# Kernel tuning notes

Measured on AMD Instinct MI355X. Metric: run time of the kernel, lower is better.

The kernel has to match this reference:

```python
import jax, jax.numpy as jnp
import numpy as np
from math import ceil, log2

LEVELS = 6
N = 4096
DB4 = np.array([0.23037781330885523, 0.7148465705525415, 0.6308807679295904,
                -0.02798376941698385, -0.18703481171888114, 0.030841381835986965,
                0.032883011666982945, -0.010597401784997278], dtype=np.float32)


def setup_inputs() -> dict:
    key = jax.random.key(0)
    x = jax.random.normal(key, (N, N), dtype=jnp.float32)
    # learned filter bank: scaling.repeat(levels*2, 1)
    scaling = jnp.tile(jnp.asarray(DB4), (LEVELS * 2, 1))
    return {
        "x": x,
        "scaling": scaling,
        "alpha": jnp.float32(10.0),
        "b_plus": jnp.float32(2.0),
        "b_minus": jnp.float32(1.0),
    }


def compute_wavelet(h):
    # g_k = flip(h); odd indices negated
    g = jnp.flip(h, -1)
    sign = jnp.where(jnp.arange(g.shape[-1]) % 2 == 1, -1.0, 1.0).astype(g.dtype)
    return g * sign


def convolve(x, f, transpose=False):
    # circular convolution (or correlation if transpose) along last axis via FFT,
    # exactly as torch rfft/irfft with n=input_length
    L = x.shape[-1]
    fa = jnp.fft.rfft(x, axis=-1)
    fb = jnp.fft.rfft(f, n=L)
    if transpose:
        fb = jnp.conj(fb)
    return jnp.fft.irfft(fa * fb, n=L, axis=-1)


def forward_layer(x, h):
    w = compute_wavelet(h)
    return convolve(x, w)[:, ::2], convolve(x, h)[:, ::2]


def backward_layer(d, a, h):
    w = compute_wavelet(h)
    fd = jnp.zeros((d.shape[0], d.shape[1] * 2), d.dtype).at[:, ::2].set(d)
    fa = jnp.zeros((a.shape[0], a.shape[1] * 2), a.dtype).at[:, ::2].set(a)
    return convolve(fd, w, transpose=True) + convolve(fa, h, transpose=True)


def forward2d(x, hH, hV):
    d, a = forward_layer(x, hH)
    hh, hl = forward_layer(d.T, hV)
    hh, hl = hh.T, hl.T
    lh, ll = forward_layer(a.T, hV)
    lh, ll = lh.T, ll.T
    return (hh, hl, lh), ll


def backward2d(hh, hl, lh, ll, hH, hV):
    h = backward_layer(hh.T, hl.T, hV).T
    l = backward_layer(lh.T, ll.T, hV).T
    return backward_layer(h, l, hH)


def _despawn(x, scaling, alpha, b_plus, b_minus):
    n, m = x.shape
    pn = 2 ** ceil(log2(n)) - n
    pm = 2 ** ceil(log2(m)) - m
    xp = jnp.pad(x, ((0, pn), (0, pm)), mode="edge") if (pn or pm) else x

    approx = xp
    coeffs = []
    for lev in range(LEVELS):
        dets, approx = forward2d(approx, scaling[lev], scaling[lev + 1])
        coeffs.append(dets)

    def thr(t):
        return t * (jax.nn.sigmoid(alpha * (t - b_plus)) + jax.nn.sigmoid(-alpha * (t + b_minus)))

    filt = [tuple(thr(c) for c in tup) for tup in coeffs] + [thr(approx)]

    a = filt[-1]
    for lev in reversed(range(LEVELS)):
        hh, hl, lh = filt[lev]
        a = backward2d(hh, hl, lh, a, scaling[lev], scaling[lev + 1])

    flat = jnp.concatenate(
        [jnp.concatenate(tup, axis=-1).reshape(-1) for tup in filt[:-1]]
        + [filt[-1].reshape(-1)]
    )
    return a[:n, :m], flat


def reference(x, scaling, alpha, b_plus, b_minus):
    return _despawn(x, scaling, alpha, b_plus, b_minus)
```

## Files before the change

### kernel.cpp

```cpp
#include <hip/hip_runtime.h>


__device__ __forceinline__ float thrf(float t, float alpha, float bp, float bm) {
    float s1 = 1.0f / (1.0f + __expf(-alpha * (t - bp)));
    float s2 = 1.0f / (1.0f + __expf( alpha * (t + bm)));
    return t * (s1 + s2);
}

__device__ __forceinline__ void load_filt(const float* __restrict__ filt,
                                          float (&h)[8], float (&w)[8]) {
#pragma unroll
    for (int k = 0; k < 8; ++k) h[k] = filt[k];
#pragma unroll
    for (int k = 0; k < 8; ++k) w[k] = (k & 1) ? -h[7 - k] : h[7 - k];
}

__global__ __launch_bounds__(256) void fwd_fused(
    const float* __restrict__ X, int s, int sh,
    float* __restrict__ flat, float* __restrict__ All,
    const float* __restrict__ filt_row, const float* __restrict__ filt_col,
    const float* __restrict__ ap, const float* __restrict__ bpp,
    const float* __restrict__ bmp) {
    __shared__ __align__(16) float xs[70][72];
    __shared__ __align__(16) float Ds[70][36];
    __shared__ __align__(16) float As[70][36];
    const int tid = threadIdx.x;
    const int j0 = blockIdx.x * 32, i0 = blockIdx.y * 32;
    float hr[8], wr[8], hc[8], wc[8];
    load_filt(filt_row, hr, wr);
    load_filt(filt_col, hc, wc);
    const int sm = s - 1;

    for (int idx = tid; idx < 70 * 18; idx += 256) {
        int rr = idx / 18, c = idx - rr * 18;
        int gr = (2 * i0 - 7 + rr) & sm;
        int gc = (2 * j0 - 8 + 4 * c) & sm;
        *(float4*)&xs[rr][4 * c] = *(const float4*)&X[(size_t)gr * s + gc];
    }
    __syncthreads();

    for (int idx = tid; idx < 70 * 8; idx += 256) {
        int rr = idx >> 3, q = idx & 7;
        const float4* xr = (const float4*)&xs[rr][8 * q];
        float wv[16];
#pragma unroll
        for (int m = 0; m < 4; ++m) {
            float4 t = xr[m];
            wv[4 * m + 0] = t.x; wv[4 * m + 1] = t.y;
            wv[4 * m + 2] = t.z; wv[4 * m + 3] = t.w;
        }
        float d[4], a[4];
#pragma unroll
        for (int e = 0; e < 4; ++e) {
            float dd = 0.f, aa = 0.f;
#pragma unroll
            for (int u = 0; u < 8; ++u) {
                float v = wv[2 * e + 1 + u];
                dd += wr[7 - u] * v;
                aa += hr[7 - u] * v;
            }
            d[e] = dd; a[e] = aa;
        }
        *(float4*)&Ds[rr][4 * q] = make_float4(d[0], d[1], d[2], d[3]);
        *(float4*)&As[rr][4 * q] = make_float4(a[0], a[1], a[2], a[3]);
    }
    __syncthreads();

    const float alpha = *ap, bp = *bpp, bm = *bmp;
    {
        const int j = tid & 31, iq = tid >> 5;
        float Dw[14], Aw[14];
#pragma unroll
        for (int t = 0; t < 14; ++t) {
            Dw[t] = Ds[8 * iq + t][j];
            Aw[t] = As[8 * iq + t][j];
        }
#pragma unroll
        for (int e = 0; e < 4; ++e) {
            float hh = 0.f, hl = 0.f, lh = 0.f, ll = 0.f;
#pragma unroll
            for (int u = 0; u < 8; ++u) {
                float dv = Dw[2 * e + u], av = Aw[2 * e + u];
                hh += wc[7 - u] * dv;
                hl += hc[7 - u] * dv;
                lh += wc[7 - u] * av;
                ll += hc[7 - u] * av;
            }
            int row = i0 + 4 * iq + e;
            size_t ro = (size_t)row * (3 * sh) + (j0 + j);
            flat[ro]           = thrf(hh, alpha, bp, bm);
            flat[ro + sh]      = thrf(hl, alpha, bp, bm);
            flat[ro + 2 * sh]  = thrf(lh, alpha, bp, bm);
            All[(size_t)row * sh + (j0 + j)] = ll;
        }
    }
}

__global__ void thr_kernel(const float* __restrict__ in, float* __restrict__ out,
                           int n, const float* __restrict__ ap,
                           const float* __restrict__ bpp,
                           const float* __restrict__ bmp) {
    int idx = blockIdx.x * blockDim.x + threadIdx.x;
    if (idx >= n) return;
    out[idx] = thrf(in[idx], *ap, *bpp, *bmp);
}

__global__ __launch_bounds__(256) void inv_fused(
    const float* __restrict__ flatl, const float* __restrict__ a, int astride,
    int sc, float* __restrict__ outp, int ostride,
    const float* __restrict__ filt_col, const float* __restrict__ filt_row) {
    __shared__ __align__(16) float hhs[36][36], hls[36][36], lhs[36][36], as_[36][36];
    __shared__ __align__(16) float Hs[64][36], Ls[64][36];
    const int tid = threadIdx.x;
    const int m0 = blockIdx.x * 64, i0 = blockIdx.y * 64;
    float hr[8], wr[8], hc[8], wc[8];
    load_filt(filt_row, hr, wr);
    load_filt(filt_col, hc, wc);
    const int mm = sc - 1;
    const int r0 = i0 >> 1, c0 = m0 >> 1;
    const int ds = 3 * sc;

    for (int idx = tid; idx < 4 * 324; idx += 256) {
        int aid = idx / 324, rem = idx - aid * 324;
        int rr = rem / 9, c = rem - rr * 9;
        int gr = (r0 + rr) & mm;
        int gc = (c0 + 4 * c) & mm;
        if (aid == 0)
            *(float4*)&hhs[rr][4 * c] = *(const float4*)&flatl[(size_t)gr * ds + gc];
        else if (aid == 1)
            *(float4*)&hls[rr][4 * c] = *(const float4*)&flatl[(size_t)gr * ds + sc + gc];
        else if (aid == 2)
            *(float4*)&lhs[rr][4 * c] = *(const float4*)&flatl[(size_t)gr * ds + 2 * sc + gc];
        else
            *(float4*)&as_[rr][4 * c] = *(const float4*)&a[(size_t)gr * astride + gc];
    }
    __syncthreads();

    for (int idx = tid; idx < 16 * 36; idx += 256) {
        int q = idx / 36, jj = idx - q * 36;
        float hv[6], lv[6], gv[6], av[6];
#pragma unroll
        for (int d = 0; d < 6; ++d) {
            int lr = 2 * q + d;
            hv[d] = hhs[lr][jj];
            lv[d] = hls[lr][jj];
            gv[d] = lhs[lr][jj];
            av[d] = as_[lr][jj];
        }
        float H0 = 0.f, H1 = 0.f, H2 = 0.f, H3 = 0.f;
        float L0 = 0.f, L1 = 0.f, L2 = 0.f, L3 = 0.f;
#pragma unroll
        for (int t = 0; t < 4; ++t) {
            float we = wc[2 * t], he = hc[2 * t];
            float wo = wc[2 * t + 1], ho = hc[2 * t + 1];
            H0 += we * hv[t]     + he * lv[t];
            H1 += wo * hv[t + 1] + ho * lv[t + 1];
            H2 += we * hv[t + 1] + he * lv[t + 1];
            H3 += wo * hv[t + 2] + ho * lv[t + 2];
            L0 += we * gv[t]     + he * av[t];
            L1 += wo * gv[t + 1] + ho * av[t + 1];
            L2 += we * gv[t + 1] + he * av[t + 1];
            L3 += wo * gv[t + 2] + ho * av[t + 2];
        }
        Hs[4 * q + 0][jj] = H0; Hs[4 * q + 1][jj] = H1;
        Hs[4 * q + 2][jj] = H2; Hs[4 * q + 3][jj] = H3;
        Ls[4 * q + 0][jj] = L0; Ls[4 * q + 1][jj] = L1;
        Ls[4 * q + 2][jj] = L2; Ls[4 * q + 3][jj] = L3;
    }
    __syncthreads();

    for (int idx = tid; idx < 64 * 16; idx += 256) {
        int i = idx >> 4, p = idx & 15;
        const float2* hp = (const float2*)&Hs[i][2 * p];
        const float2* lp = (const float2*)&Ls[i][2 * p];
        float2 hA = hp[0], hB = hp[1], hC = hp[2];
        float2 lA = lp[0], lB = lp[1], lC = lp[2];
        float Hw[6] = {hA.x, hA.y, hB.x, hB.y, hC.x, hC.y};
        float Lw[6] = {lA.x, lA.y, lB.x, lB.y, lC.x, lC.y};
        float o0 = 0.f, o1 = 0.f, o2 = 0.f, o3 = 0.f;
#pragma unroll
        for (int t = 0; t < 4; ++t) {
            float we = wr[2 * t], he = hr[2 * t];
            float wo = wr[2 * t + 1], ho = hr[2 * t + 1];
            o0 += we * Hw[t]     + he * Lw[t];
            o1 += wo * Hw[t + 1] + ho * Lw[t + 1];
            o2 += we * Hw[t + 1] + he * Lw[t + 1];
            o3 += wo * Hw[t + 2] + ho * Lw[t + 2];
        }
        *(float4*)&outp[(size_t)(i0 + i) * ostride + (m0 + 4 * p)] =
            make_float4(o0, o1, o2, o3);
    }
}

extern "C" void kernel_launch(void* const* d_in, const int* in_sizes, int n_in,
                              void* d_out, int out_size, void* d_ws, size_t ws_size,
                              hipStream_t stream) {
    const float* x    = (const float*)d_in[0];
    const float* scal = (const float*)d_in[1];
    const float* ap   = (const float*)d_in[2];
    const float* bp   = (const float*)d_in[3];
    const float* bm   = (const float*)d_in[4];
    float* out = (float*)d_out;
    float* ws  = (float*)d_ws;

    const int N = 4096;
    float* recon = out;
    float* flat  = out + 16777216;

    static const size_t Aoff[7] = {0, 0, 4194304, 5242880, 5505024, 5570560, 5586944};
    static const size_t flatOff[6] = {0, 12582912, 15728640, 16515072, 16711680, 16760832};
    const size_t finalOff = 16773120;
    float* P0 = ws + 5591040;
    float* P1 = ws + 5591040 + 4194304;

    dim3 blk(256);

    const float* src = x;
    for (int lev = 0; lev < 6; ++lev) {
        int s = N >> lev, sh = s >> 1;
        dim3 g(sh / 32, sh / 32);
        fwd_fused<<<g, blk, 0, stream>>>(src, s, sh, flat + flatOff[lev],
                                         ws + Aoff[lev + 1],
                                         scal + lev * 8, scal + (lev + 1) * 8,
                                         ap, bp, bm);
        src = ws + Aoff[lev + 1];
    }
    thr_kernel<<<dim3(16), blk, 0, stream>>>(ws + Aoff[6], flat + finalOff, 4096,
                                             ap, bp, bm);

    const float* a_in = flat + finalOff;
    for (int lev = 5; lev >= 0; --lev) {
        int sc = N >> (lev + 1), r = 2 * sc;
        float* outp = (lev == 0) ? recon : ((lev & 1) ? P1 : P0);
        dim3 g(r / 64, r / 64);
        inv_fused<<<g, blk, 0, stream>>>(flat + flatOff[lev], a_in, sc,
                                         sc, outp, r,
                                         scal + (lev + 1) * 8, scal + lev * 8);
        a_in = outp;
    }
}
```

Baseline: 307.0 us.

## Drop input shared-memory staging, fuse final threshold, split passes to cut registers

Both kernels now read their input windows straight from global memory instead of staging them in shared memory. This shrinks LDS use, and __launch_bounds__(256,8) is added to raise occupancy. The column passes are split into two halves so fewer register arrays are live at once. Wavelet coefficients are derived inline from h rather than kept in separate registers, and the final-approx threshold is folded into the last forward kernel, which removes one launch. The cost is redundant global/L2 reads of overlapping halos and less-coalesced scalar loads in the inverse kernel.

```diff
diff --git a/kernel.cpp b/kernel.cpp
--- a/kernel.cpp
+++ b/kernel.cpp
@@ -7,45 +7,30 @@
     return t * (s1 + s2);
 }
 
-__device__ __forceinline__ void load_filt(const float* __restrict__ filt,
-                                          float (&h)[8], float (&w)[8]) {
+__device__ __forceinline__ void load_h(const float* __restrict__ filt,
+                                       float (&h)[8]) {
 #pragma unroll
     for (int k = 0; k < 8; ++k) h[k] = filt[k];
-#pragma unroll
-    for (int k = 0; k < 8; ++k) w[k] = (k & 1) ? -h[7 - k] : h[7 - k];
-}
-
-__global__ __launch_bounds__(256) void fwd_fused(
-    const float* __restrict__ X, int s, int sh,
-    float* __restrict__ flat, float* __restrict__ All,
-    const float* __restrict__ filt_row, const float* __restrict__ filt_col,
-    const float* __restrict__ ap, const float* __restrict__ bpp,
-    const float* __restrict__ bmp) {
-    __shared__ __align__(16) float xs[70][72];
-    __shared__ __align__(16) float Ds[70][36];
-    __shared__ __align__(16) float As[70][36];
-    const int tid = threadIdx.x;
-    const int j0 = blockIdx.x * 32, i0 = blockIdx.y * 32;
-    float hr[8], wr[8], hc[8], wc[8];
-    load_filt(filt_row, hr, wr);
-    load_filt(filt_col, hc, wc);
-    const int sm = s - 1;
-
-    for (int idx = tid; idx < 70 * 18; idx += 256) {
-        int rr = idx / 18, c = idx - rr * 18;
-        int gr = (2 * i0 - 7 + rr) & sm;
-        int gc = (2 * j0 - 8 + 4 * c) & sm;
-        *(float4*)&xs[rr][4 * c] = *(const float4*)&X[(size_t)gr * s + gc];
-    }
-    __syncthreads();
-
+}
+
+struct SMemF { float Ds[70][36]; float As[70][36]; };
+struct SMemI { float Hs[64][36]; float Ls[64][36]; };
+
+__device__ __forceinline__ void fwd_tile(
+    SMemF& sm, const float* __restrict__ X, int s, int sh,
+    float* __restrict__ flat, float* __restrict__ All, bool thr_ll,
+    const float (&h)[8], const float (&g)[8],
+    float alpha, float bp, float bm, int i0, int j0, int tid) {
+    const int smk = s - 1;
     for (int idx = tid; idx < 70 * 8; idx += 256) {
         int rr = idx >> 3, q = idx & 7;
-        const float4* xr = (const float4*)&xs[rr][8 * q];
+        int gr = (2 * i0 - 7 + rr) & smk;
+        const float* xrow = X + (size_t)gr * s;
+        int cbase = 2 * j0 - 8 + 8 * q;
         float wv[16];
 #pragma unroll
         for (int m = 0; m < 4; ++m) {
-            float4 t = xr[m];
+            float4 t = *(const float4*)&xrow[(cbase + 4 * m) & smk];
             wv[4 * m + 0] = t.x; wv[4 * m + 1] = t.y;
             wv[4 * m + 2] = t.z; wv[4 * m + 3] = t.w;
         }
@@ -56,123 +41,116 @@
 #pragma unroll
             for (int u = 0; u < 8; ++u) {
                 float v = wv[2 * e + 1 + u];
-                dd += wr[7 - u] * v;
-                aa += hr[7 - u] * v;
+                aa += h[7 - u] * v;
+                dd += (u & 1) ? h[u] * v : -h[u] * v;
             }
             d[e] = dd; a[e] = aa;
         }
-        *(float4*)&Ds[rr][4 * q] = make_float4(d[0], d[1], d[2], d[3]);
-        *(float4*)&As[rr][4 * q] = make_float4(a[0], a[1], a[2], a[3]);
+        *(float4*)&sm.Ds[rr][4 * q] = make_float4(d[0], d[1], d[2], d[3]);
+        *(float4*)&sm.As[rr][4 * q] = make_float4(a[0], a[1], a[2], a[3]);
     }
     __syncthreads();
-
-    const float alpha = *ap, bp = *bpp, bm = *bmp;
+    const int j = tid & 31, iq = tid >> 5;
     {
-        const int j = tid & 31, iq = tid >> 5;
-        float Dw[14], Aw[14];
-#pragma unroll
-        for (int t = 0; t < 14; ++t) {
-            Dw[t] = Ds[8 * iq + t][j];
-            Aw[t] = As[8 * iq + t][j];
-        }
+        float Dw[14];
+#pragma unroll
+        for (int t = 0; t < 14; ++t) Dw[t] = sm.Ds[8 * iq + t][j];
 #pragma unroll
         for (int e = 0; e < 4; ++e) {
-            float hh = 0.f, hl = 0.f, lh = 0.f, ll = 0.f;
+            float hh = 0.f, hl = 0.f;
 #pragma unroll
             for (int u = 0; u < 8; ++u) {
-                float dv = Dw[2 * e + u], av = Aw[2 * e + u];
-                hh += wc[7 - u] * dv;
-                hl += hc[7 - u] * dv;
-                lh += wc[7 - u] * av;
-                ll += hc[7 - u] * av;
+                float dv = Dw[2 * e + u];
+                hl += g[7 - u] * dv;
+                hh += (u & 1) ? g[u] * dv : -g[u] * dv;
             }
             int row = i0 + 4 * iq + e;
             size_t ro = (size_t)row * (3 * sh) + (j0 + j);
-            flat[ro]           = thrf(hh, alpha, bp, bm);
-            flat[ro + sh]      = thrf(hl, alpha, bp, bm);
-            flat[ro + 2 * sh]  = thrf(lh, alpha, bp, bm);
-            All[(size_t)row * sh + (j0 + j)] = ll;
-        }
-    }
-}
-
-__global__ void thr_kernel(const float* __restrict__ in, float* __restrict__ out,
-                           int n, const float* __restrict__ ap,
-                           const float* __restrict__ bpp,
-                           const float* __restrict__ bmp) {
-    int idx = blockIdx.x * blockDim.x + threadIdx.x;
-    if (idx >= n) return;
-    out[idx] = thrf(in[idx], *ap, *bpp, *bmp);
-}
-
-__global__ __launch_bounds__(256) void inv_fused(
-    const float* __restrict__ flatl, const float* __restrict__ a, int astride,
-    int sc, float* __restrict__ outp, int ostride,
-    const float* __restrict__ filt_col, const float* __restrict__ filt_row) {
-    __shared__ __align__(16) float hhs[36][36], hls[36][36], lhs[36][36], as_[36][36];
-    __shared__ __align__(16) float Hs[64][36], Ls[64][36];
-    const int tid = threadIdx.x;
-    const int m0 = blockIdx.x * 64, i0 = blockIdx.y * 64;
-    float hr[8], wr[8], hc[8], wc[8];
-    load_filt(filt_row, hr, wr);
-    load_filt(filt_col, hc, wc);
+            flat[ro]      = thrf(hh, alpha, bp, bm);
+            flat[ro + sh] = thrf(hl, alpha, bp, bm);
+        }
+    }
+    {
+        float Aw[14];
+#pragma unroll
+        for (int t = 0; t < 14; ++t) Aw[t] = sm.As[8 * iq + t][j];
+#pragma unroll
+        for (int e = 0; e < 4; ++e) {
+            float lh = 0.f, ll = 0.f;
+#pragma unroll
+            for (int u = 0; u < 8; ++u) {
+                float av = Aw[2 * e + u];
+                ll += g[7 - u] * av;
+                lh += (u & 1) ? g[u] * av : -g[u] * av;
+            }
+            int row = i0 + 4 * iq + e;
+            size_t ro = (size_t)row * (3 * sh) + (j0 + j);
+            flat[ro + 2 * sh] = thrf(lh, alpha, bp, bm);
+            All[(size_t)row * sh + (j0 + j)] =
+                thr_ll ? thrf(ll, alpha, bp, bm) : ll;
+        }
+    }
+}
+
+__device__ __forceinline__ void inv_tile(
+    SMemI& sm, const float* __restrict__ flatl, const float* __restrict__ a,
+    int astride, int sc, float* __restrict__ outp, int ostride,
+    const float (&h)[8], const float (&g)[8],
+    int i0, int m0, int tid) {
     const int mm = sc - 1;
     const int r0 = i0 >> 1, c0 = m0 >> 1;
     const int ds = 3 * sc;
-
-    for (int idx = tid; idx < 4 * 324; idx += 256) {
-        int aid = idx / 324, rem = idx - aid * 324;
-        int rr = rem / 9, c = rem - rr * 9;
-        int gr = (r0 + rr) & mm;
-        int gc = (c0 + 4 * c) & mm;
-        if (aid == 0)
-            *(float4*)&hhs[rr][4 * c] = *(const float4*)&flatl[(size_t)gr * ds + gc];
-        else if (aid == 1)
-            *(float4*)&hls[rr][4 * c] = *(const float4*)&flatl[(size_t)gr * ds + sc + gc];
-        else if (aid == 2)
-            *(float4*)&lhs[rr][4 * c] = *(const float4*)&flatl[(size_t)gr * ds + 2 * sc + gc];
-        else
-            *(float4*)&as_[rr][4 * c] = *(const float4*)&a[(size_t)gr * astride + gc];
-    }
-    __syncthreads();
-
     for (int idx = tid; idx < 16 * 36; idx += 256) {
         int q = idx / 36, jj = idx - q * 36;
-        float hv[6], lv[6], gv[6], av[6];
-#pragma unroll
-        for (int d = 0; d < 6; ++d) {
-            int lr = 2 * q + d;
-            hv[d] = hhs[lr][jj];
-            lv[d] = hls[lr][jj];
-            gv[d] = lhs[lr][jj];
-            av[d] = as_[lr][jj];
-        }
-        float H0 = 0.f, H1 = 0.f, H2 = 0.f, H3 = 0.f;
-        float L0 = 0.f, L1 = 0.f, L2 = 0.f, L3 = 0.f;
-#pragma unroll
-        for (int t = 0; t < 4; ++t) {
-            float we = wc[2 * t], he = hc[2 * t];
-            float wo = wc[2 * t + 1], ho = hc[2 * t + 1];
-            H0 += we * hv[t]     + he * lv[t];
-            H1 += wo * hv[t + 1] + ho * lv[t + 1];
-            H2 += we * hv[t + 1] + he * lv[t + 1];
-            H3 += wo * hv[t + 2] + ho * lv[t + 2];
-            L0 += we * gv[t]     + he * av[t];
-            L1 += wo * gv[t + 1] + ho * av[t + 1];
-            L2 += we * gv[t + 1] + he * av[t + 1];
-            L3 += wo * gv[t + 2] + ho * av[t + 2];
-        }
-        Hs[4 * q + 0][jj] = H0; Hs[4 * q + 1][jj] = H1;
-        Hs[4 * q + 2][jj] = H2; Hs[4 * q + 3][jj] = H3;
-        Ls[4 * q + 0][jj] = L0; Ls[4 * q + 1][jj] = L1;
-        Ls[4 * q + 2][jj] = L2; Ls[4 * q + 3][jj] = L3;
+        int gc = (c0 + jj) & mm;
+        {
+            float hv[6], lv[6];
+#pragma unroll
+            for (int d = 0; d < 6; ++d) {
+                size_t o = (size_t)((r0 + 2 * q + d) & mm) * ds + gc;
+                hv[d] = flatl[o];
+                lv[d] = flatl[o + sc];
+            }
+            float H0 = 0.f, H1 = 0.f, H2 = 0.f, H3 = 0.f;
+#pragma unroll
+            for (int t = 0; t < 4; ++t) {
+                float we = g[7 - 2 * t], wo = -g[6 - 2 * t];
+                float he = g[2 * t],     ho = g[2 * t + 1];
+                H0 += we * hv[t]     + he * lv[t];
+                H1 += wo * hv[t + 1] + ho * lv[t + 1];
+                H2 += we * hv[t + 1] + he * lv[t + 1];
+                H3 += wo * hv[t + 2] + ho * lv[t + 2];
+            }
+            sm.Hs[4 * q + 0][jj] = H0; sm.Hs[4 * q + 1][jj] = H1;
+            sm.Hs[4 * q + 2][jj] = H2; sm.Hs[4 * q + 3][jj] = H3;
+        }
+        {
+            float gv[6], av[6];
+#pragma unroll
+            for (int d = 0; d < 6; ++d) {
+                int grr = (r0 + 2 * q + d) & mm;
+                gv[d] = flatl[(size_t)grr * ds + 2 * sc + gc];
+                av[d] = a[(size_t)grr * astride + gc];
+            }
+            float L0 = 0.f, L1 = 0.f, L2 = 0.f, L3 = 0.f;
+#pragma unroll
+            for (int t = 0; t < 4; ++t) {
+                float we = g[7 - 2 * t], wo = -g[6 - 2 * t];
+                float he = g[2 * t],     ho = g[2 * t + 1];
+                L0 += we * gv[t]     + he * av[t];
+                L1 += wo * gv[t + 1] + ho * av[t + 1];
+                L2 += we * gv[t + 1] + he * av[t + 1];
+                L3 += wo * gv[t + 2] + ho * av[t + 2];
+            }
+            sm.Ls[4 * q + 0][jj] = L0; sm.Ls[4 * q + 1][jj] = L1;
+            sm.Ls[4 * q + 2][jj] = L2; sm.Ls[4 * q + 3][jj] = L3;
+        }
     }
     __syncthreads();
-
     for (int idx = tid; idx < 64 * 16; idx += 256) {
         int i = idx >> 4, p = idx & 15;
-        const float2* hp = (const float2*)&Hs[i][2 * p];
-        const float2* lp = (const float2*)&Ls[i][2 * p];
+        const float2* hp = (const float2*)&sm.Hs[i][2 * p];
+        const float2* lp = (const float2*)&sm.Ls[i][2 * p];
         float2 hA = hp[0], hB = hp[1], hC = hp[2];
         float2 lA = lp[0], lB = lp[1], lC = lp[2];
         float Hw[6] = {hA.x, hA.y, hB.x, hB.y, hC.x, hC.y};
@@ -180,8 +158,8 @@
         float o0 = 0.f, o1 = 0.f, o2 = 0.f, o3 = 0.f;
 #pragma unroll
         for (int t = 0; t < 4; ++t) {
-            float we = wr[2 * t], he = hr[2 * t];
-            float wo = wr[2 * t + 1], ho = hr[2 * t + 1];
+            float we = h[7 - 2 * t], wo = -h[6 - 2 * t];
+            float he = h[2 * t],     ho = h[2 * t + 1];
             o0 += we * Hw[t]     + he * Lw[t];
             o1 += wo * Hw[t + 1] + ho * Lw[t + 1];
             o2 += we * Hw[t + 1] + he * Lw[t + 1];
@@ -190,6 +168,33 @@
         *(float4*)&outp[(size_t)(i0 + i) * ostride + (m0 + 4 * p)] =
             make_float4(o0, o1, o2, o3);
     }
+}
+
+__global__ __launch_bounds__(256, 8) void fwd_fused(
+    const float* __restrict__ X, int s, int sh,
+    float* __restrict__ flat, float* __restrict__ All, int thr_ll,
+    const float* __restrict__ filt_row, const float* __restrict__ filt_col,
+    const float* __restrict__ ap, const float* __restrict__ bpp,
+    const float* __restrict__ bmp) {
+    __shared__ SMemF smem;
+    float h[8], g[8];
+    load_h(filt_row, h);
+    load_h(filt_col, g);
+    const float alpha = *ap, bp = *bpp, bm = *bmp;
+    fwd_tile(smem, X, s, sh, flat, All, thr_ll != 0, h, g,
+             alpha, bp, bm, blockIdx.y * 32, blockIdx.x * 32, threadIdx.x);
+}
+
+__global__ __launch_bounds__(256, 8) void inv_fused(
+    const float* __restrict__ flatl, const float* __restrict__ a, int astride,
+    int sc, float* __restrict__ outp, int ostride,
+    const float* __restrict__ filt_col, const float* __restrict__ filt_row) {
+    __shared__ SMemI smem;
+    float h[8], g[8];
+    load_h(filt_row, h);
+    load_h(filt_col, g);
+    inv_tile(smem, flatl, a, astride, sc, outp, ostride, h, g,
+             blockIdx.y * 64, blockIdx.x * 64, threadIdx.x);
 }
 
 extern "C" void kernel_launch(void* const* d_in, const int* in_sizes, int n_in,
@@ -206,8 +211,7 @@
     const int N = 4096;
     float* recon = out;
     float* flat  = out + 16777216;
-
-    static const size_t Aoff[7] = {0, 0, 4194304, 5242880, 5505024, 5570560, 5586944};
+    static const size_t Aoff[7]    = {0, 0, 4194304, 5242880, 5505024, 5570560, 5586944};
     static const size_t flatOff[6] = {0, 12582912, 15728640, 16515072, 16711680, 16760832};
     const size_t finalOff = 16773120;
     float* P0 = ws + 5591040;
@@ -219,14 +223,13 @@
     for (int lev = 0; lev < 6; ++lev) {
         int s = N >> lev, sh = s >> 1;
         dim3 g(sh / 32, sh / 32);
-        fwd_fused<<<g, blk, 0, stream>>>(src, s, sh, flat + flatOff[lev],
-                                         ws + Aoff[lev + 1],
+        float* All = (lev < 5) ? (ws + Aoff[lev + 1]) : (flat + finalOff);
+        fwd_fused<<<g, blk, 0, stream>>>(src, s, sh, flat + flatOff[lev], All,
+                                         (lev == 5) ? 1 : 0,
                                          scal + lev * 8, scal + (lev + 1) * 8,
                                          ap, bp, bm);
         src = ws + Aoff[lev + 1];
     }
-    thr_kernel<<<dim3(16), blk, 0, stream>>>(ws + Aoff[6], flat + finalOff, 4096,
-                                             ap, bp, bm);
 
     const float* a_in = flat + finalOff;
     for (int lev = 5; lev >= 0; --lev) {
```

Measured after the change: 287.7 us. 1.07x faster.
